# Optimization experiments

Measured on AMD Instinct MI355X. Metric: run time of the kernel, lower is better.

## Reference

```python
import jax, jax.numpy as jnp
import numpy as np

MID = 256

def setup_inputs() -> dict:
    key = jax.random.key(0)
    ks = jax.random.split(key, 6)
    s = 1.0 / np.sqrt(MID)
    u = lambda k, shape: jax.random.uniform(k, shape, jnp.float32, -s, s)
    return {
        "W_ih": u(ks[0], (4 * MID, 2)),
        "W_hh": u(ks[1], (4 * MID, MID)),
        "b_ih": u(ks[2], (4 * MID,)),
        "b_hh": u(ks[3], (4 * MID,)),
        "W_out": u(ks[4], (1, MID)),
        "b_out": u(ks[5], (1,)),
        "sequence_dim": 48,
        "sequence_num": 512,
    }

def reference(W_ih, W_hh, b_ih, b_hh, W_out, b_out, sequence_dim, sequence_num):
    # obs is 2-D -> torch nn.LSTM treats it as UNBATCHED: (L=sequence_num, H_in=2),
    # hidden state (mid,) per layer, carried across outer iterations.
    N = sequence_num
    mid = W_hh.shape[1]
    b = b_ih + b_hh  # fuse the two LSTM biases

    def lstm(hc, obs):
        # obs: (N, 2) time-major unbatched sequence
        def step(carry, x):
            h, c = carry
            g = W_ih @ x + W_hh @ h + b          # (4*mid,)
            i, f, gg, o = jnp.split(g, 4)         # torch gate order i,f,g,o
            c = jax.nn.sigmoid(f) * c + jax.nn.sigmoid(i) * jnp.tanh(gg)
            h = jax.nn.sigmoid(o) * jnp.tanh(c)
            return (h, c), h
        hc, hs = jax.lax.scan(step, hc, obs)
        return hc, hs                              # hs: (N, mid)

    def outer(carry, k):
        hc, samp, prob = carry
        obs = jnp.concatenate([samp, prob], axis=1)  # (N, 2)
        hc, hs = lstm(hc, obs)
        p = jax.nn.sigmoid(hs @ W_out.T + b_out)     # (N, 1)
        smp = jax.random.bernoulli(k, p).astype(p.dtype)
        lp = smp * jnp.log(p) + (1.0 - smp) * jnp.log1p(-p)        # Bernoulli log_prob
        ent = -(p * jnp.log(p) + (1.0 - p) * jnp.log1p(-p))        # Bernoulli entropy
        return (hc, smp, p), (smp[:, 0], lp[:, 0], ent[:, 0])

    key = jax.random.key(42)
    keys = jax.random.split(key, sequence_dim - 1)
    h0 = (jnp.zeros((mid,), W_hh.dtype), jnp.zeros((mid,), W_hh.dtype))
    z = jnp.zeros((N, 1), W_hh.dtype)
    _, (ss, lps, ents) = jax.lax.scan(outer, (h0, z, z), keys)

    samples = jnp.concatenate([jnp.zeros((1, N), ss.dtype), ss], axis=0)  # (T, N)
    samples = samples.T.astype(jnp.int32)                                  # (N, T)
    logprobs = lps.sum(0)
    logprobs = logprobs - logprobs.mean()
    entropies = ents.mean(0)
    return samples, logprobs, entropies
```

## Files before the change

### kernel.cpp

```cpp
#include <hip/hip_runtime.h>
#include <stdint.h>


#define MID      256
#define NOUT     48
#define NSEQ     512
#define NOUTER   47
#define NSTEP    (NOUTER * NSEQ)
#define NWRK     16
#define SAMP_BLK 16
#define MAGIC_V  0x1234ABCDu
#define LOG2E    1.4426950408889634f

#define AL_RELAX(p)    __hip_atomic_load((p), __ATOMIC_RELAXED, __HIP_MEMORY_SCOPE_AGENT)
#define AL_ACQ(p)      __hip_atomic_load((p), __ATOMIC_ACQUIRE, __HIP_MEMORY_SCOPE_AGENT)
#define AS_RELAX(p, v) __hip_atomic_store((p), (v), __ATOMIC_RELAXED, __HIP_MEMORY_SCOPE_AGENT)
#define AS_REL(p, v)   __hip_atomic_store((p), (v), __ATOMIC_RELEASE, __HIP_MEMORY_SCOPE_AGENT)

__device__ __forceinline__ uint32_t rotl32(uint32_t x, int d) {
  return (x << d) | (x >> (32 - d));
}

__device__ __forceinline__ void threefry2x32(uint32_t k0, uint32_t k1,
                                             uint32_t x0, uint32_t x1,
                                             uint32_t& o0, uint32_t& o1) {
  uint32_t ks2 = k0 ^ k1 ^ 0x1BD11BDAu;
  uint32_t v0 = x0 + k0, v1 = x1 + k1;
#define TF_R(r) { v0 += v1; v1 = rotl32(v1, r); v1 ^= v0; }
  TF_R(13) TF_R(15) TF_R(26) TF_R(6)
  v0 += k1;  v1 += ks2 + 1u;
  TF_R(17) TF_R(29) TF_R(16) TF_R(24)
  v0 += ks2; v1 += k0 + 2u;
  TF_R(13) TF_R(15) TF_R(26) TF_R(6)
  v0 += k0;  v1 += k1 + 3u;
  TF_R(17) TF_R(29) TF_R(16) TF_R(24)
  v0 += k1;  v1 += ks2 + 4u;
  TF_R(13) TF_R(15) TF_R(26) TF_R(6)
  v0 += ks2; v1 += k0 + 5u;
#undef TF_R
  o0 = v0; o1 = v1;
}

__device__ __forceinline__ float sigf(float x) { return 1.0f / (1.0f + expf(-x)); }

__device__ __forceinline__ float fsig(float x) {
  return __builtin_amdgcn_rcpf(1.0f + __builtin_amdgcn_exp2f(x * (-LOG2E)));
}
__device__ __forceinline__ float ftanh(float x) {
  const float e = __builtin_amdgcn_exp2f(x * (-2.0f * LOG2E));
  return __builtin_fmaf(2.0f, __builtin_amdgcn_rcpf(1.0f + e), -1.0f);
}

template <int CTRL>
__device__ __forceinline__ float dpp_xadd(float x) {
  int v = __builtin_amdgcn_update_dpp(0, __float_as_int(x), CTRL, 0xF, 0xF, true);
  return x + __int_as_float(v);
}

__device__ __forceinline__ uint64_t packht(float h, uint32_t tag) {
  return ((uint64_t)tag << 32) | (uint64_t)__float_as_uint(h);
}

__global__ __launch_bounds__(256, 1)
void arlstm_kernel(const float* __restrict__ W_ih, const float* __restrict__ W_hh,
                   const float* __restrict__ b_ih, const float* __restrict__ b_hh,
                   const float* __restrict__ W_out, const float* __restrict__ b_out,
                   float* __restrict__ out, uint64_t* __restrict__ ws) {
  uint64_t* h_hist = ws;
  float*    obsbuf = (float*)(ws + 512 * 256);
  uint32_t* p_prog = (uint32_t*)(obsbuf + 2 * 512 * 2);
  uint32_t* magic  = p_prog + 16;

  const int tid = threadIdx.x;
  const int blk = blockIdx.x;

  __shared__ __align__(16) float hstp[2 * 292];
  __shared__ float obs_s[4];
  __shared__ float lp_acc[512];
  __shared__ float ent_acc[512];
  __shared__ float red[256];

  if (blk == SAMP_BLK) {
    AS_RELAX(&h_hist[tid], 0ull);
    if (tid < 16) AS_RELAX(&p_prog[tid], 0u);
    out[(tid)       * NOUT] = 0.0f;
    out[(tid + 256) * NOUT] = 0.0f;
    lp_acc[tid] = 0.0f;  lp_acc[tid + 256] = 0.0f;
    ent_acc[tid] = 0.0f; ent_acc[tid + 256] = 0.0f;
    __threadfence();
    __syncthreads();
    if (tid == 0) AS_REL(magic, MAGIC_V);

    const int w    = tid >> 6;
    const int lane = tid & 63;
    const float wo0 = W_out[lane * 4 + 0], wo1 = W_out[lane * 4 + 1];
    const float wo2 = W_out[lane * 4 + 2], wo3 = W_out[lane * 4 + 3];
    const float bo = b_out[0];

    for (int s = w + 1; s <= NSTEP; s += 4) {
      const int k = (s - 1) >> 9;
      const int t = (s - 1) & 511;
      uint64_t* src = h_hist + (uint64_t)(s & 511) * 256 + lane * 4;
      uint64_t v0, v1, v2, v3;
      for (;;) {
        v0 = AL_RELAX(src + 0);
        v1 = AL_RELAX(src + 1);
        v2 = AL_RELAX(src + 2);
        v3 = AL_RELAX(src + 3);
        int ok = ((uint32_t)(v0 >> 32) == (uint32_t)s) &
                 ((uint32_t)(v1 >> 32) == (uint32_t)s) &
                 ((uint32_t)(v2 >> 32) == (uint32_t)s) &
                 ((uint32_t)(v3 >> 32) == (uint32_t)s);
        if (__all(ok)) break;
      }
      float zp = fmaf(__uint_as_float((uint32_t)v0), wo0,
                 fmaf(__uint_as_float((uint32_t)v1), wo1,
                 fmaf(__uint_as_float((uint32_t)v2), wo2,
                      __uint_as_float((uint32_t)v3) * wo3)));
      zp += __shfl_xor(zp, 1);
      zp += __shfl_xor(zp, 2);
      zp += __shfl_xor(zp, 4);
      zp += __shfl_xor(zp, 8);
      zp += __shfl_xor(zp, 16);
      zp += __shfl_xor(zp, 32);
      const float p = sigf(zp + bo);

      uint32_t ka, kb, c1, c2;
      threefry2x32(0u, 42u, 0u, (uint32_t)k, ka, kb);
      threefry2x32(ka, kb, 0u, (uint32_t)t, c1, c2);
      const uint32_t bits = c1 ^ c2;
      const float u = __uint_as_float((bits >> 9) | 0x3f800000u) - 1.0f;
      const float smp = (u < p) ? 1.0f : 0.0f;

      if (lane == 0) {
        uint32_t* ob = (uint32_t*)(obsbuf + ((k + 1) & 1) * (512 * 2) + t * 2);
        AS_RELAX(&ob[0], __float_as_uint(smp));
        AS_RELAX(&ob[1], __float_as_uint(p));
        AS_REL(&p_prog[w], (uint32_t)s);
        out[t * NOUT + (k + 1)] = smp;
        const float lg = logf(p), lg1 = log1pf(-p);
        lp_acc[t]  += (smp > 0.5f) ? lg : lg1;
        ent_acc[t] -= (p * lg + (1.0f - p) * lg1);
      }
    }
    __syncthreads();
    red[tid] = lp_acc[tid] + lp_acc[tid + 256];
    __syncthreads();
    for (int off = 128; off > 0; off >>= 1) {
      if (tid < off) red[tid] += red[tid + off];
      __syncthreads();
    }
    const float mean = red[0] * (1.0f / 512.0f);
    out[24576 + tid]        = lp_acc[tid]        - mean;
    out[24576 + 256 + tid]  = lp_acc[tid + 256]  - mean;
    out[25088 + tid]        = ent_acc[tid]       * (1.0f / 47.0f);
    out[25088 + 256 + tid]  = ent_acc[tid + 256] * (1.0f / 47.0f);
    return;
  }

  const int wv = tid >> 6;
  const int l  = tid & 63;
  const int ch = l & 7;
  const int rp = l >> 3;
  const int g  = rp >> 1;
  const int jpair = rp & 1;
  const int R0 = g * 256 + blk * 16 + wv * 4 + 2 * jpair;

  float4 w0[8], w1[8];
#pragma unroll
  for (int i = 0; i < 8; ++i) {
    w0[i] = ((const float4*)(W_hh + (uint64_t)R0 * 256 + ch * 32))[i];
    w1[i] = ((const float4*)(W_hh + (uint64_t)(R0 + 1) * 256 + ch * 32))[i];
  }

  float eb[4] = {0, 0, 0, 0}, ew0[4] = {0, 0, 0, 0}, ew1[4] = {0, 0, 0, 0};
  if (l < 4) {
#pragma unroll
    for (int g4 = 0; g4 < 4; ++g4) {
      const int rr = g4 * 256 + blk * 16 + wv * 4 + l;
      eb[g4]  = b_ih[rr] + b_hh[rr];
      ew0[g4] = W_ih[rr * 2 + 0];
      ew1[g4] = W_ih[rr * 2 + 1];
    }
  }

  while (AL_ACQ(magic) != MAGIC_V) {}

  float c_st = 0.0f;
  const int hidx = blk * 16 + wv * 4 + l;

  for (int s = 1; s <= NSTEP; ++s) {
    const int k = (s - 1) >> 9;
    const int t = (s - 1) & 511;
    const int buf = s & 1;

    if (tid == 255) {
      float sxf = 0.0f, pxf = 0.0f;
      if (k > 0) {
        const uint32_t X = (uint32_t)((k - 1) * 512 + t + 1);
        while (AL_ACQ(&p_prog[t & 3]) < X) {}
        uint32_t* ob = (uint32_t*)(obsbuf + (k & 1) * (512 * 2) + t * 2);
        sxf = __uint_as_float(AL_RELAX(&ob[0]));
        pxf = __uint_as_float(AL_RELAX(&ob[1]));
      }
      obs_s[buf * 2 + 0] = sxf;
      obs_s[buf * 2 + 1] = pxf;
    }

    {
      uint64_t* src = h_hist + (uint64_t)((s - 1) & 511) * 256 + tid;
      const uint32_t want = (uint32_t)(s - 1);
      uint64_t x = AL_RELAX(src);
      if ((uint32_t)(x >> 32) != want) {
        uint64_t y = AL_RELAX(src);
        for (;;) {
          if ((uint32_t)(x >> 32) == want) break;
          x = AL_RELAX(src);
          if ((uint32_t)(y >> 32) == want) { x = y; break; }
          y = AL_RELAX(src);
        }
      }
      hstp[buf * 292 + (tid >> 5) * 36 + (tid & 31)] = __uint_as_float((uint32_t)x);
    }
    __asm__ volatile("s_waitcnt lgkmcnt(0)" ::: "memory");
    __builtin_amdgcn_s_barrier();

    const float4* hs = (const float4*)&hstp[buf * 292 + ch * 36];
    float a00 = 0.f, a01 = 0.f, a02 = 0.f, a03 = 0.f;
    float a10 = 0.f, a11 = 0.f, a12 = 0.f, a13 = 0.f;
#pragma unroll
    for (int i = 0; i < 8; ++i) {
      const float4 hv = hs[i];
      a00 = fmaf(w0[i].x, hv.x, a00);
      a01 = fmaf(w0[i].y, hv.y, a01);
      a02 = fmaf(w0[i].z, hv.z, a02);
      a03 = fmaf(w0[i].w, hv.w, a03);
      a10 = fmaf(w1[i].x, hv.x, a10);
      a11 = fmaf(w1[i].y, hv.y, a11);
      a12 = fmaf(w1[i].z, hv.z, a12);
      a13 = fmaf(w1[i].w, hv.w, a13);
    }
    float d0 = (a00 + a01) + (a02 + a03);
    float d1 = (a10 + a11) + (a12 + a13);

    d0 = dpp_xadd<0xB1>(d0); d1 = dpp_xadd<0xB1>(d1);
    d0 = dpp_xadd<0x4E>(d0); d1 = dpp_xadd<0x4E>(d1);
    d0 += __shfl_xor(d0, 4, 64);
    d1 += __shfl_xor(d1, 4, 64);

    const int hsel = (l >> 1) & 1;
    const int osel = l & 1;
    float G0, G1, G2, G3;
    {
      const float u0 = __shfl(d0, (0 + hsel) * 8, 64);
      const float v0 = __shfl(d1, (0 + hsel) * 8, 64);
      G0 = osel ? v0 : u0;
      const float u1 = __shfl(d0, (2 + hsel) * 8, 64);
      const float v1 = __shfl(d1, (2 + hsel) * 8, 64);
      G1 = osel ? v1 : u1;
      const float u2 = __shfl(d0, (4 + hsel) * 8, 64);
      const float v2 = __shfl(d1, (4 + hsel) * 8, 64);
      G2 = osel ? v2 : u2;
      const float u3 = __shfl(d0, (6 + hsel) * 8, 64);
      const float v3 = __shfl(d1, (6 + hsel) * 8, 64);
      G3 = osel ? v3 : u3;
    }

    const float sx = obs_s[buf * 2 + 0];
    const float px = obs_s[buf * 2 + 1];
    G0 += fmaf(ew0[0], sx, fmaf(ew1[0], px, eb[0]));
    G1 += fmaf(ew0[1], sx, fmaf(ew1[1], px, eb[1]));
    G2 += fmaf(ew0[2], sx, fmaf(ew1[2], px, eb[2]));
    G3 += fmaf(ew0[3], sx, fmaf(ew1[3], px, eb[3]));
    const float gi = fsig(G0);
    const float gf = fsig(G1);
    const float gz = ftanh(G2);
    const float go = fsig(G3);
    c_st = fmaf(gf, c_st, gi * gz);
    const float hnew = go * ftanh(c_st);
    if (l < 4)
      AS_RELAX(&h_hist[(uint64_t)(s & 511) * 256 + hidx],
               packht(hnew, (uint32_t)s));
  }
}

extern "C" void kernel_launch(void* const* d_in, const int* in_sizes, int n_in,
                              void* d_out, int out_size, void* d_ws, size_t ws_size,
                              hipStream_t stream) {
  const float* W_ih  = (const float*)d_in[0];
  const float* W_hh  = (const float*)d_in[1];
  const float* b_ih  = (const float*)d_in[2];
  const float* b_hh  = (const float*)d_in[3];
  const float* W_out = (const float*)d_in[4];
  const float* b_out = (const float*)d_in[5];
  float* out = (float*)d_out;
  uint64_t* ws = (uint64_t*)d_ws;

  arlstm_kernel<<<dim3(NWRK + 1), dim3(256), 0, stream>>>(
      W_ih, W_hh, b_ih, b_hh, W_out, b_out, out, ws);
}
```

Before: 38.43 ms.

## Split K-dimension across waves and reduce LSTM gates through LDS

Each wave now owns a 64-wide slice of the hidden vector and computes partial dot products for all 64 gate rows of the block. Partials are combined through a shared-memory buffer after a second barrier, and the first 64 threads apply the activations while 16 threads update the cell state. This replaces the cross-lane shuffle reduction and gate gather, and the h polling loop now keeps four loads in flight. The trade-off is an extra block barrier on every recurrent step, which sits on the serial critical path.

```diff
diff --git a/kernel.cpp b/kernel.cpp
--- a/kernel.cpp
+++ b/kernel.cpp
@@ -43,14 +43,6 @@
 
 __device__ __forceinline__ float sigf(float x) { return 1.0f / (1.0f + expf(-x)); }
 
-__device__ __forceinline__ float fsig(float x) {
-  return __builtin_amdgcn_rcpf(1.0f + __builtin_amdgcn_exp2f(x * (-LOG2E)));
-}
-__device__ __forceinline__ float ftanh(float x) {
-  const float e = __builtin_amdgcn_exp2f(x * (-2.0f * LOG2E));
-  return __builtin_fmaf(2.0f, __builtin_amdgcn_rcpf(1.0f + e), -1.0f);
-}
-
 template <int CTRL>
 __device__ __forceinline__ float dpp_xadd(float x) {
   int v = __builtin_amdgcn_update_dpp(0, __float_as_int(x), CTRL, 0xF, 0xF, true);
@@ -60,6 +52,8 @@
 __device__ __forceinline__ uint64_t packht(float h, uint32_t tag) {
   return ((uint64_t)tag << 32) | (uint64_t)__float_as_uint(h);
 }
+
+#define BARRIER_LGKM() __asm__ volatile("s_waitcnt lgkmcnt(0)\ns_barrier" ::: "memory")
 
 __global__ __launch_bounds__(256, 1)
 void arlstm_kernel(const float* __restrict__ W_ih, const float* __restrict__ W_hh,
@@ -74,7 +68,8 @@
   const int tid = threadIdx.x;
   const int blk = blockIdx.x;
 
-  __shared__ __align__(16) float hstp[2 * 292];
+  __shared__ __align__(16) float hstage[256];
+  __shared__ float plds[4][64];
   __shared__ float obs_s[4];
   __shared__ float lp_acc[512];
   __shared__ float ent_acc[512];
@@ -160,39 +155,39 @@
 
   const int wv = tid >> 6;
   const int l  = tid & 63;
-  const int ch = l & 7;
-  const int rp = l >> 3;
-  const int g  = rp >> 1;
-  const int jpair = rp & 1;
-  const int R0 = g * 256 + blk * 16 + wv * 4 + 2 * jpair;
+  const int hf = l & 1;
+  const int lr = l & ~1;
+  const int gr0 = ((lr)     >> 4) * 256 + blk * 16 + ((lr)     & 15);
+  const int gr1 = ((lr + 1) >> 4) * 256 + blk * 16 + ((lr + 1) & 15);
 
   float4 w0[8], w1[8];
 #pragma unroll
   for (int i = 0; i < 8; ++i) {
-    w0[i] = ((const float4*)(W_hh + (uint64_t)R0 * 256 + ch * 32))[i];
-    w1[i] = ((const float4*)(W_hh + (uint64_t)(R0 + 1) * 256 + ch * 32))[i];
-  }
-
-  float eb[4] = {0, 0, 0, 0}, ew0[4] = {0, 0, 0, 0}, ew1[4] = {0, 0, 0, 0};
-  if (l < 4) {
-#pragma unroll
-    for (int g4 = 0; g4 < 4; ++g4) {
-      const int rr = g4 * 256 + blk * 16 + wv * 4 + l;
-      eb[g4]  = b_ih[rr] + b_hh[rr];
-      ew0[g4] = W_ih[rr * 2 + 0];
-      ew1[g4] = W_ih[rr * 2 + 1];
-    }
+    w0[i] = ((const float4*)(W_hh + (uint64_t)gr0 * 256 + wv * 64 + hf * 32))[i];
+    w1[i] = ((const float4*)(W_hh + (uint64_t)gr1 * 256 + wv * 64 + hf * 32))[i];
+  }
+
+  float bb = 0.f, wx0 = 0.f, wx1 = 0.f, mconst = 0.f, ml = 0.f, ad = 0.f;
+  if (tid < 64) {
+    const int g4 = tid >> 4;
+    const int rr = g4 * 256 + blk * 16 + (tid & 15);
+    bb  = b_ih[rr] + b_hh[rr];
+    wx0 = W_ih[rr * 2 + 0];
+    wx1 = W_ih[rr * 2 + 1];
+    mconst = (g4 == 2) ? (-2.0f * LOG2E) : (-LOG2E);
+    ml     = (g4 == 2) ? 2.0f : 1.0f;
+    ad     = (g4 == 2) ? -1.0f : 0.0f;
   }
 
   while (AL_ACQ(magic) != MAGIC_V) {}
 
   float c_st = 0.0f;
-  const int hidx = blk * 16 + wv * 4 + l;
+  const int jglob = blk * 16 + (tid & 15);
 
   for (int s = 1; s <= NSTEP; ++s) {
     const int k = (s - 1) >> 9;
     const int t = (s - 1) & 511;
-    const int buf = s & 1;
+    const int par = s & 1;
 
     if (tid == 255) {
       float sxf = 0.0f, pxf = 0.0f;
@@ -203,29 +198,31 @@
         sxf = __uint_as_float(AL_RELAX(&ob[0]));
         pxf = __uint_as_float(AL_RELAX(&ob[1]));
       }
-      obs_s[buf * 2 + 0] = sxf;
-      obs_s[buf * 2 + 1] = pxf;
+      obs_s[par * 2 + 0] = sxf;
+      obs_s[par * 2 + 1] = pxf;
     }
 
     {
       uint64_t* src = h_hist + (uint64_t)((s - 1) & 511) * 256 + tid;
       const uint32_t want = (uint32_t)(s - 1);
-      uint64_t x = AL_RELAX(src);
-      if ((uint32_t)(x >> 32) != want) {
-        uint64_t y = AL_RELAX(src);
-        for (;;) {
-          if ((uint32_t)(x >> 32) == want) break;
-          x = AL_RELAX(src);
-          if ((uint32_t)(y >> 32) == want) { x = y; break; }
-          y = AL_RELAX(src);
-        }
-      }
-      hstp[buf * 292 + (tid >> 5) * 36 + (tid & 31)] = __uint_as_float((uint32_t)x);
-    }
-    __asm__ volatile("s_waitcnt lgkmcnt(0)" ::: "memory");
-    __builtin_amdgcn_s_barrier();
-
-    const float4* hs = (const float4*)&hstp[buf * 292 + ch * 36];
+      uint64_t x0 = AL_RELAX(src), x1 = AL_RELAX(src);
+      uint64_t x2 = AL_RELAX(src), x3 = AL_RELAX(src);
+      uint64_t v;
+      for (;;) {
+        if ((uint32_t)(x0 >> 32) == want) { v = x0; break; }
+        x0 = AL_RELAX(src);
+        if ((uint32_t)(x1 >> 32) == want) { v = x1; break; }
+        x1 = AL_RELAX(src);
+        if ((uint32_t)(x2 >> 32) == want) { v = x2; break; }
+        x2 = AL_RELAX(src);
+        if ((uint32_t)(x3 >> 32) == want) { v = x3; break; }
+        x3 = AL_RELAX(src);
+      }
+      hstage[tid] = __uint_as_float((uint32_t)v);
+    }
+    BARRIER_LGKM();
+
+    const float4* hs = (const float4*)(hstage + wv * 64 + hf * 32);
     float a00 = 0.f, a01 = 0.f, a02 = 0.f, a03 = 0.f;
     float a10 = 0.f, a11 = 0.f, a12 = 0.f, a13 = 0.f;
 #pragma unroll
@@ -242,45 +239,34 @@
     }
     float d0 = (a00 + a01) + (a02 + a03);
     float d1 = (a10 + a11) + (a12 + a13);
-
-    d0 = dpp_xadd<0xB1>(d0); d1 = dpp_xadd<0xB1>(d1);
-    d0 = dpp_xadd<0x4E>(d0); d1 = dpp_xadd<0x4E>(d1);
-    d0 += __shfl_xor(d0, 4, 64);
-    d1 += __shfl_xor(d1, 4, 64);
-
-    const int hsel = (l >> 1) & 1;
-    const int osel = l & 1;
-    float G0, G1, G2, G3;
-    {
-      const float u0 = __shfl(d0, (0 + hsel) * 8, 64);
-      const float v0 = __shfl(d1, (0 + hsel) * 8, 64);
-      G0 = osel ? v0 : u0;
-      const float u1 = __shfl(d0, (2 + hsel) * 8, 64);
-      const float v1 = __shfl(d1, (2 + hsel) * 8, 64);
-      G1 = osel ? v1 : u1;
-      const float u2 = __shfl(d0, (4 + hsel) * 8, 64);
-      const float v2 = __shfl(d1, (4 + hsel) * 8, 64);
-      G2 = osel ? v2 : u2;
-      const float u3 = __shfl(d0, (6 + hsel) * 8, 64);
-      const float v3 = __shfl(d1, (6 + hsel) * 8, 64);
-      G3 = osel ? v3 : u3;
-    }
-
-    const float sx = obs_s[buf * 2 + 0];
-    const float px = obs_s[buf * 2 + 1];
-    G0 += fmaf(ew0[0], sx, fmaf(ew1[0], px, eb[0]));
-    G1 += fmaf(ew0[1], sx, fmaf(ew1[1], px, eb[1]));
-    G2 += fmaf(ew0[2], sx, fmaf(ew1[2], px, eb[2]));
-    G3 += fmaf(ew0[3], sx, fmaf(ew1[3], px, eb[3]));
-    const float gi = fsig(G0);
-    const float gf = fsig(G1);
-    const float gz = ftanh(G2);
-    const float go = fsig(G3);
-    c_st = fmaf(gf, c_st, gi * gz);
-    const float hnew = go * ftanh(c_st);
-    if (l < 4)
-      AS_RELAX(&h_hist[(uint64_t)(s & 511) * 256 + hidx],
-               packht(hnew, (uint32_t)s));
+    d0 = dpp_xadd<0xB1>(d0);
+    d1 = dpp_xadd<0xB1>(d1);
+    plds[wv][l] = hf ? d1 : d0;
+    BARRIER_LGKM();
+
+    if (tid < 64) {
+      const float sx = obs_s[par * 2 + 0];
+      const float px = obs_s[par * 2 + 1];
+      const float gv = ((plds[0][tid] + plds[1][tid]) +
+                        (plds[2][tid] + plds[3][tid])) +
+                       fmaf(wx0, sx, fmaf(wx1, px, bb));
+      const float e   = __builtin_amdgcn_exp2f(gv * mconst);
+      const float y   = __builtin_amdgcn_rcpf(1.0f + e);
+      const float act = __builtin_fmaf(ml, y, ad);
+      const int j = tid & 15;
+      const float a_f = __shfl(act, j + 16, 64);
+      const float a_g = __shfl(act, j + 32, 64);
+      const float a_o = __shfl(act, j + 48, 64);
+      if (tid < 16) {
+        c_st = fmaf(a_f, c_st, act * a_g);
+        const float ec = __builtin_amdgcn_exp2f(c_st * (-2.0f * LOG2E));
+        const float yc = __builtin_amdgcn_rcpf(1.0f + ec);
+        const float th = __builtin_fmaf(2.0f, yc, -1.0f);
+        const float hnew = a_o * th;
+        AS_RELAX(&h_hist[(uint64_t)(s & 511) * 256 + jglob],
+                 packht(hnew, (uint32_t)s));
+      }
+    }
   }
 }
 
```

After: 36.61 ms. -4.8%, faster.
